# Kernel tuning notes

Measured on AMD Instinct MI355X. Metric: run time of the kernel, lower is better.

The kernel has to match this reference:

```python
import jax, jax.numpy as jnp
import numpy as np
import math

L = 2      # num_patient_encoder_layers
NE = 4     # number of note-type experts
H = 768    # hidden_size
FF = 4 * H # dim_feedforward
NH = H // 64  # num heads
HD = 64       # head dim
B, S = 8, 256
EPS = 1e-5


def setup_inputs() -> dict:
    key = jax.random.key(0)
    ks = jax.random.split(key, 12)
    std = 0.02
    x = jax.random.normal(ks[0], (B, S, H), dtype=jnp.float32)
    # all notes valid; note_pos values are 1..B*S so order_notes is an identity permutation
    note_pos = (jnp.arange(B * S, dtype=jnp.int64) + 1).reshape(B, S)
    note_type_pos = jax.random.randint(ks[1], (B * S,), 0, NE)
    Wq = jax.random.normal(ks[2], (L, H, H), dtype=jnp.float32) * std
    Wk = jax.random.normal(ks[3], (L, H, H), dtype=jnp.float32) * std
    Wv = jax.random.normal(ks[4], (L, H, H), dtype=jnp.float32) * std
    bq = jnp.zeros((L, H), jnp.float32)
    bk = jnp.zeros((L, H), jnp.float32)
    bv = jnp.zeros((L, H), jnp.float32)
    ln1_w = jnp.ones((L, H), jnp.float32)
    ln1_b = jnp.zeros((L, H), jnp.float32)
    ln2_w = jnp.ones((L, H), jnp.float32)
    ln2_b = jnp.zeros((L, H), jnp.float32)
    W1 = jax.random.normal(ks[5], (L, NE, H, FF), dtype=jnp.float32) * std
    b1 = jnp.zeros((L, NE, FF), jnp.float32)
    W2 = jax.random.normal(ks[6], (L, NE, FF, H), dtype=jnp.float32) * std
    b2 = jnp.zeros((L, NE, H), jnp.float32)
    return dict(x=x, note_pos=note_pos, note_type_pos=note_type_pos,
                Wq=Wq, bq=bq, Wk=Wk, bk=bk, Wv=Wv, bv=bv,
                ln1_w=ln1_w, ln1_b=ln1_b, ln2_w=ln2_w, ln2_b=ln2_b,
                W1=W1, b1=b1, W2=W2, b2=b2)


def _layer_norm(x, w, b):
    mu = jnp.mean(x, axis=-1, keepdims=True)
    var = jnp.mean(jnp.square(x - mu), axis=-1, keepdims=True)
    return (x - mu) * jax.lax.rsqrt(var + EPS) * w + b


def _sinusoidal_pe(seq_len, d_model):
    pos = jnp.arange(seq_len, dtype=jnp.float32)[:, None]
    div = jnp.exp(jnp.arange(0, d_model, 2, dtype=jnp.float32) * (-math.log(10000.0) / d_model))
    ang = pos * div  # [S, H/2]
    # interleave sin at even, cos at odd indices
    return jnp.stack([jnp.sin(ang), jnp.cos(ang)], axis=-1).reshape(seq_len, d_model)


def reference(x, note_pos, note_type_pos, Wq, bq, Wk, bk, Wv, bv,
              ln1_w, ln1_b, ln2_w, ln2_b, W1, b1, W2, b2):
    Bc, Sc, Hc = x.shape
    x = x + _sinusoidal_pe(Sc, Hc)[None]
    attn_mask = (note_pos != 0).astype(x.dtype)                 # [B, S]
    add_mask = (1.0 - attn_mask)[:, None, None, :] * -10000.0    # [B,1,1,S]
    flat_idx = note_pos.reshape(-1)                              # identity perm, values 1..B*S

    for l in range(L):
        # --- self attention (no 1/sqrt(d) scaling, as in source) ---
        h = _layer_norm(x, ln1_w[l], ln1_b[l])
        q = (h @ Wq[l] + bq[l]).reshape(Bc, Sc, NH, HD)
        k = (h @ Wk[l] + bk[l]).reshape(Bc, Sc, NH, HD)
        v = (h @ Wv[l] + bv[l]).reshape(Bc, Sc, NH, HD)
        scores = jnp.einsum('bqhd,bkhd->bhqk', q, k) + add_mask
        probs = jax.nn.softmax(scores, axis=-1)
        ctx = jnp.einsum('bhqk,bkhd->bqhd', probs, v).reshape(Bc, Sc, Hc)
        x = x + ctx

        # --- gather valid notes to flat token list (identity here) ---
        xf = x.reshape(-1, Hc)                                   # [T, H]
        hf = _layer_norm(xf, ln2_w[l], ln2_b[l])
        # --- note-type routed expert FFN ---
        out = jnp.zeros_like(xf)
        for e in range(NE):
            he = jax.nn.gelu(hf @ W1[l, e] + b1[l, e], approximate=False) @ W2[l, e] + b2[l, e]
            out = jnp.where((note_type_pos == e)[:, None], he, out)
        xf = xf + out
        # --- scatter back via order_notes: pad zero row, gather by note_pos ---
        padded = jnp.concatenate([jnp.zeros((1, Hc), xf.dtype), xf], axis=0)
        x = padded[flat_idx].reshape(Bc, Sc, Hc)
    return x
```

## Files before the change

### kernel.cpp

```cpp
#include <hip/hip_runtime.h>

typedef __bf16 bf16_t;
typedef __attribute__((ext_vector_type(8))) __bf16 bf16x8;
typedef __attribute__((ext_vector_type(4))) float f32x4;

static constexpr int Lc = 2, NEc = 4, Hc = 768, FFc = 3072, NHc = 12;
static constexpr int Bc = 8, Tc = 2048;

__device__ __forceinline__ void gll16(const bf16_t* g, bf16_t* l) {
  __builtin_amdgcn_global_load_lds(
      (const __attribute__((address_space(1))) void*)g,
      (__attribute__((address_space(3))) void*)l, 16, 0, 0);
}

__global__ __launch_bounds__(64) void route_k(const int* __restrict__ ntp,
                                              int* __restrict__ perm,
                                              int* __restrict__ offs) {
  int lane = threadIdx.x;
  int myE[32];
  int cnt0 = 0, cnt1 = 0, cnt2 = 0, cnt3 = 0;
  for (int c = 0; c < 32; ++c) {
    int e = ntp[c * 64 + lane];
    myE[c] = e;
    cnt0 += __popcll(__ballot(e == 0));
    cnt1 += __popcll(__ballot(e == 1));
    cnt2 += __popcll(__ballot(e == 2));
    cnt3 += __popcll(__ballot(e == 3));
  }
  int b0 = 0, b1 = cnt0, b2 = cnt0 + cnt1, b3 = cnt0 + cnt1 + cnt2;
  if (lane == 0) {
    offs[0] = 0; offs[1] = b1; offs[2] = b2; offs[3] = b3; offs[4] = b3 + cnt3;
  }
  unsigned long long below = (lane == 63) ? ~0ull >> 1 : ((1ull << lane) - 1);
  for (int c = 0; c < 32; ++c) {
    int e = myE[c];
    unsigned long long m0 = __ballot(e == 0), m1 = __ballot(e == 1);
    unsigned long long m2 = __ballot(e == 2), m3 = __ballot(e == 3);
    unsigned long long mm = (e == 0) ? m0 : (e == 1) ? m1 : (e == 2) ? m2 : m3;
    int base = (e == 0) ? b0 : (e == 1) ? b1 : (e == 2) ? b2 : b3;
    perm[base + __popcll(mm & below)] = c * 64 + lane;
    b0 += __popcll(m0); b1 += __popcll(m1); b2 += __popcll(m2); b3 += __popcll(m3);
  }
}

__global__ __launch_bounds__(256) void pe_add(const float* __restrict__ xin,
                                              float* __restrict__ x0) {
  int p = blockIdx.x * 256 + threadIdx.x;
  int t = p / 384;
  int jj = p - t * 384;
  int s = t & 255;
  float ang = (float)s * __expf((float)jj * -0.0239852613894f);
  float sn, cs;
  sincosf(ang, &sn, &cs);
  float2 xv = ((const float2*)xin)[p];
  float2 o;  o.x = xv.x + sn;  o.y = xv.y + cs;
  ((float2*)x0)[p] = o;
}

__global__ __launch_bounds__(256) void ln_k(const float* __restrict__ x,
                                            const float* __restrict__ g,
                                            const float* __restrict__ bb,
                                            bf16_t* __restrict__ out) {
  int w = threadIdx.x >> 6, lane = threadIdx.x & 63;
  int t = blockIdx.x * 4 + w;
  const float4* xr = (const float4*)(x + (size_t)t * Hc);
  float4 v[3];
  float s = 0.f, s2 = 0.f;
  for (int i = 0; i < 3; ++i) {
    v[i] = xr[lane + i * 64];
    s  += v[i].x + v[i].y + v[i].z + v[i].w;
    s2 += v[i].x * v[i].x + v[i].y * v[i].y + v[i].z * v[i].z + v[i].w * v[i].w;
  }
  for (int o = 1; o < 64; o <<= 1) { s += __shfl_xor(s, o); s2 += __shfl_xor(s2, o); }
  float mu = s * (1.f / 768.f);
  float r = rsqrtf(s2 * (1.f / 768.f) - mu * mu + 1e-5f);
  bf16_t* orow = out + (size_t)t * Hc;
  for (int i = 0; i < 3; ++i) {
    int i4 = lane + i * 64;
    float4 gg = ((const float4*)g)[i4];
    float4 b4 = ((const float4*)bb)[i4];
    union { bf16_t h[4]; uint2 u; } pk;
    pk.h[0] = (bf16_t)((v[i].x - mu) * r * gg.x + b4.x);
    pk.h[1] = (bf16_t)((v[i].y - mu) * r * gg.y + b4.y);
    pk.h[2] = (bf16_t)((v[i].z - mu) * r * gg.z + b4.z);
    pk.h[3] = (bf16_t)((v[i].w - mu) * r * gg.w + b4.w);
    ((uint2*)orow)[i4] = pk.u;
  }
}

__global__ __launch_bounds__(256) void tconv(const float* __restrict__ s0,
                                             const float* __restrict__ s1,
                                             const float* __restrict__ s2,
                                             int mdiv, long sls, long sms,
                                             bf16_t* __restrict__ dst, long dls, long dms,
                                             int K, int N) {
  int z = blockIdx.z;
  int l = z / mdiv, m = z % mdiv;
  const float* src;
  if (s1) src = (m == 0 ? s0 : (m == 1 ? s1 : s2)) + (size_t)l * sls;
  else src = s0 + (size_t)l * sls + (size_t)m * sms;
  bf16_t* d = dst + (size_t)l * dls + (size_t)m * dms;
  int n0 = blockIdx.x * 64, k0 = blockIdx.y * 64;
  __shared__ float tl[64][65];
  int c = threadIdx.x & 63, r0 = threadIdx.x >> 6;
  for (int i = 0; i < 16; ++i) {
    int r = r0 + i * 4;
    tl[r][c] = src[(size_t)(k0 + r) * N + n0 + c];
  }
  __syncthreads();
  for (int i = 0; i < 16; ++i) {
    int r = r0 + i * 4;
    d[(size_t)(n0 + r) * K + k0 + c] = (bf16_t)tl[c][r];
  }
}

template <int MODE, int BM>
__global__ __launch_bounds__(256) void gemm2(
    const bf16_t* __restrict__ A, const bf16_t* __restrict__ Bt,
    int K, int N, int kIters, long btStride, long biasStride,
    const int* __restrict__ perm, const int* __restrict__ offs,
    const float* __restrict__ bqp, const float* __restrict__ bkp,
    const float* __restrict__ bvp, const float* __restrict__ biasE,
    float* __restrict__ outF, bf16_t* __restrict__ outB) {
  constexpr int TM = BM / 32;
  constexpr int TN = 2;
  constexpr int AI = BM / 32;
  __shared__ bf16_t Ald[BM * 64];
  __shared__ bf16_t Bld[64 * 64];
  int tid = threadIdx.x, lane = tid & 63, w = tid >> 6;
  int quad = lane >> 4, col = lane & 15;
  int m0 = blockIdx.y * BM, n0 = blockIdx.x * 64;
  int e = 0, ks = 0, kStart = 0, off = 0, cnt = Tc;
  if (MODE == 1) e = blockIdx.z;
  if (MODE == 2) { e = blockIdx.z >> 1; ks = blockIdx.z & 1; kStart = ks * (K / 2); }
  if (MODE != 0) {
    off = offs[e];
    cnt = offs[e + 1] - off;
    if (m0 >= cnt) return;
  }
  const bf16_t* B0 = Bt + (size_t)e * btStride;

  const bf16_t* ga[AI];
  bf16_t* la[AI];
  for (int j = 0; j < AI; ++j) {
    int rbase = w * (BM / 4) + j * 8;
    int row = rbase + (lane >> 3);
    int ch = ((lane & 7) - row) & 7;
    int gm = m0 + row;
    int gmc = (gm < cnt) ? gm : (cnt - 1);
    int srow;
    if (MODE == 0) srow = gm;
    else if (MODE == 1) srow = perm[off + gmc];
    else srow = off + gmc;
    ga[j] = A + (size_t)srow * K + kStart + ch * 8;
    la[j] = Ald + rbase * 64;
  }
  const bf16_t* gb[2];
  bf16_t* lb[2];
  for (int j = 0; j < 2; ++j) {
    int rbase = w * 16 + j * 8;
    int row = rbase + (lane >> 3);
    int ch = ((lane & 7) - row) & 7;
    gb[j] = B0 + (size_t)(n0 + row) * K + kStart + ch * 8;
    lb[j] = Bld + rbase * 64;
  }

  int wr = (w >> 1) * (BM / 2), wc = (w & 1) * 32;
  int aoff[TM], boff[TN];
  for (int r = 0; r < TM; ++r) {
    int row = wr + r * 16 + col;
    aoff[r] = row * 64 + (((quad + row) & 7) << 3);
  }
  for (int c = 0; c < TN; ++c) {
    int row = wc + c * 16 + col;
    boff[c] = row * 64 + (((quad + row) & 7) << 3);
  }

  const f32x4 z4 = {0.f, 0.f, 0.f, 0.f};
  f32x4 acc[TM][TN];
  for (int r = 0; r < TM; ++r)
    for (int c = 0; c < TN; ++c) acc[r][c] = z4;

  for (int it = 0; it < kIters; ++it) {
    __syncthreads();
    for (int j = 0; j < AI; ++j) gll16(ga[j], la[j]);
    for (int j = 0; j < 2; ++j) gll16(gb[j], lb[j]);
    for (int j = 0; j < AI; ++j) ga[j] += 64;
    for (int j = 0; j < 2; ++j) gb[j] += 64;
    __syncthreads();
    for (int kk = 0; kk < 2; ++kk) {
      bf16x8 af[TM], bv[TN];
      for (int r = 0; r < TM; ++r) af[r] = *(const bf16x8*)(Ald + (aoff[r] ^ (kk << 5)));
      for (int c = 0; c < TN; ++c) bv[c] = *(const bf16x8*)(Bld + (boff[c] ^ (kk << 5)));
      for (int r = 0; r < TM; ++r)
        for (int c = 0; c < TN; ++c)
          acc[r][c] = __builtin_amdgcn_mfma_f32_16x16x32_bf16(af[r], bv[c], acc[r][c], 0, 0, 0);
    }
  }

  for (int r = 0; r < TM; ++r)
    for (int c = 0; c < TN; ++c) {
      int mloc = wr + r * 16 + quad * 4;
      int n = n0 + wc + c * 16 + col;
      for (int i = 0; i < 4; ++i) {
        int gm = m0 + mloc + i;
        float av = acc[r][c][i];
        if (MODE == 0) {
          float bias = (n < 768) ? bqp[n] : (n < 1536) ? bkp[n - 768] : bvp[n - 1536];
          outB[(size_t)gm * N + n] = (bf16_t)(av + bias);
        } else if (MODE == 1) {
          if (gm < cnt) {
            float v = av + biasE[(size_t)e * biasStride + n];
            float u = v * (0.7978845608f + 0.0356774081f * v * v);
            float t = 1.f - 2.f / (1.f + __expf(2.f * u));
            outB[(size_t)(off + gm) * N + n] = (bf16_t)(0.5f * v * (1.f + t));
          }
        } else {
          if (gm < cnt) {
            int tok = perm[off + gm];
            outF[(size_t)ks * Tc * Hc + (size_t)tok * N + n] = av;
          }
        }
      }
    }
}

__global__ __launch_bounds__(256) void attn_k(const bf16_t* __restrict__ qkv,
                                              const int* __restrict__ np,
                                              float* __restrict__ x) {
  __shared__ bf16_t Kld[256 * 64];
  __shared__ bf16_t Vt[64 * 256];
  int tid = threadIdx.x, lane = tid & 63, w = tid >> 6;
  int qt = blockIdx.x;
  int b = blockIdx.y / NHc, h = blockIdx.y % NHc;

  for (int j = 0; j < 8; ++j) {
    int rbase = w * 64 + j * 8;
    int row = rbase + (lane >> 3);
    int oc = ((lane & 7) - row) & 7;
    const bf16_t* gp = qkv + ((size_t)(b * 256 + row)) * 2304 + 768 + h * 64 + oc * 8;
    gll16(gp, Kld + rbase * 64);
  }
  {
    int s = tid, shi = s >> 3, slo = s & 7;
    const uint4* vs = (const uint4*)(qkv + ((size_t)(b * 256 + s)) * 2304 + 1536 + h * 64);
    for (int cc = 0; cc < 8; ++cc) {
      uint4 pk = vs[cc];
      const bf16_t* pv = (const bf16_t*)&pk;
      for (int jj = 0; jj < 8; ++jj) {
        int d = cc * 8 + jj;
        Vt[d * 256 + ((shi + d) & 31) * 8 + slo] = pv[jj];
      }
    }
  }
  int quad = lane >> 4, col = lane & 15;
  float madd[16];
  for (int nt = 0; nt < 16; ++nt)
    madd[nt] = (np[b * 256 + nt * 16 + col] != 0) ? 0.f : -10000.f;
  int qrow = qt * 64 + w * 16 + col;
  const bf16_t* qb = qkv + ((size_t)(b * 256 + qrow)) * 2304 + h * 64;
  bf16x8 qf0 = *(const bf16x8*)(qb + quad * 8);
  bf16x8 qf1 = *(const bf16x8*)(qb + 32 + quad * 8);
  __syncthreads();

  const f32x4 z4 = {0.f, 0.f, 0.f, 0.f};
  f32x4 sc[16];
  for (int nt = 0; nt < 16; ++nt) {
    int row = nt * 16 + col;
    bf16x8 k0 = *(const bf16x8*)(Kld + row * 64 + (((0 + quad + row) & 7) << 3));
    bf16x8 k1 = *(const bf16x8*)(Kld + row * 64 + (((4 + quad + row) & 7) << 3));
    f32x4 z = z4;
    z = __builtin_amdgcn_mfma_f32_16x16x32_bf16(qf0, k0, z, 0, 0, 0);
    z = __builtin_amdgcn_mfma_f32_16x16x32_bf16(qf1, k1, z, 0, 0, 0);
    sc[nt] = z;
  }
  for (int nt = 0; nt < 16; ++nt) {
    float a = madd[nt];
    sc[nt][0] += a; sc[nt][1] += a; sc[nt][2] += a; sc[nt][3] += a;
  }
  float pm[4], rl[4];
  for (int i = 0; i < 4; ++i) {
    float m = -1e30f;
    for (int nt = 0; nt < 16; ++nt) m = fmaxf(m, sc[nt][i]);
    for (int o = 1; o < 16; o <<= 1) m = fmaxf(m, __shfl_xor(m, o));
    float ssum = 0.f;
    for (int nt = 0; nt < 16; ++nt) ssum += __expf(sc[nt][i] - m);
    for (int o = 1; o < 16; o <<= 1) ssum += __shfl_xor(ssum, o);
    pm[i] = m;
    rl[i] = 1.f / ssum;
  }
  __syncthreads();
  bf16_t* Pb = Kld + w * 4096;
  for (int nt = 0; nt < 16; ++nt)
    for (int i = 0; i < 4; ++i) {
      int prow = quad * 4 + i;
      int key = nt * 16 + col;
      Pb[prow * 256 + (((key >> 3) + prow) & 31) * 8 + (key & 7)] =
          (bf16_t)__expf(sc[nt][i] - pm[i]);
    }
  __syncthreads();
  f32x4 oacc[4];
  for (int i = 0; i < 4; ++i) oacc[i] = z4;
  for (int kk2 = 0; kk2 < 8; ++kk2) {
    bf16x8 pa = *(const bf16x8*)(Pb + col * 256 + (((kk2 * 4 + quad + col) & 31) << 3));
    for (int nt2 = 0; nt2 < 4; ++nt2) {
      int d = nt2 * 16 + col;
      bf16x8 bv8 = *(const bf16x8*)(Vt + d * 256 + (((kk2 * 4 + quad + d) & 31) << 3));
      oacc[nt2] = __builtin_amdgcn_mfma_f32_16x16x32_bf16(pa, bv8, oacc[nt2], 0, 0, 0);
    }
  }
  for (int nt2 = 0; nt2 < 4; ++nt2)
    for (int i = 0; i < 4; ++i) {
      size_t o = ((size_t)(b * 256 + qt * 64 + w * 16 + quad * 4 + i)) * Hc + h * 64 + nt2 * 16 + col;
      x[o] += oacc[nt2][i] * rl[i];
    }
}

__global__ __launch_bounds__(256) void combine_k(const float* __restrict__ x0,
                                                 const float* __restrict__ pbuf,
                                                 const float* __restrict__ b2l,
                                                 const int* __restrict__ ntp,
                                                 const int* __restrict__ np,
                                                 float* __restrict__ dst) {
  int i = blockIdx.x * 256 + threadIdx.x;
  int t = i / 192, d = i - t * 192;
  int idx = np[t];
  float4 o;
  if (idx != 0) {
    int r = idx - 1;
    int e = ntp[r];
    size_t j = (size_t)r * 192 + d;
    float4 a = ((const float4*)x0)[j];
    float4 p0 = ((const float4*)pbuf)[j];
    float4 p1 = ((const float4*)pbuf)[(size_t)Tc * 192 + j];
    float4 bb = ((const float4*)(b2l + (size_t)e * Hc))[d];
    o.x = a.x + p0.x + p1.x + bb.x;
    o.y = a.y + p0.y + p1.y + bb.y;
    o.z = a.z + p0.z + p1.z + bb.z;
    o.w = a.w + p0.w + p1.w + bb.w;
  } else {
    o.x = o.y = o.z = o.w = 0.f;
  }
  ((float4*)dst)[i] = o;
}

extern "C" void kernel_launch(void* const* d_in, const int* in_sizes, int n_in,
                              void* d_out, int out_size, void* d_ws, size_t ws_size,
                              hipStream_t stream) {
  const float* x_in = (const float*)d_in[0];
  const int* note_pos = (const int*)d_in[1];
  const int* ntp = (const int*)d_in[2];
  const float* Wq = (const float*)d_in[3];
  const float* bq = (const float*)d_in[4];
  const float* Wk = (const float*)d_in[5];
  const float* bk = (const float*)d_in[6];
  const float* Wv = (const float*)d_in[7];
  const float* bv = (const float*)d_in[8];
  const float* ln1w = (const float*)d_in[9];
  const float* ln1b = (const float*)d_in[10];
  const float* ln2w = (const float*)d_in[11];
  const float* ln2b = (const float*)d_in[12];
  const float* W1 = (const float*)d_in[13];
  const float* b1 = (const float*)d_in[14];
  const float* W2 = (const float*)d_in[15];
  const float* b2 = (const float*)d_in[16];
  float* out = (float*)d_out;

  char* p = (char*)d_ws;
  auto carve = [&](size_t bytes) -> char* {
    char* r = p;
    p += (bytes + 255) & ~(size_t)255;
    return r;
  };
  float* xA = (float*)carve((size_t)Tc * Hc * 4);
  float* xB = (float*)carve((size_t)Tc * Hc * 4);
  float* pbuf = (float*)carve((size_t)2 * Tc * Hc * 4);
  bf16_t* h16 = (bf16_t*)carve((size_t)Tc * Hc * 2);
  bf16_t* big = (bf16_t*)carve((size_t)Tc * FFc * 2);
  bf16_t* qkv16 = big;
  bf16_t* act1 = big;
  bf16_t* wqkvt = (bf16_t*)carve((size_t)Lc * 2304 * 768 * 2);
  bf16_t* w1t = (bf16_t*)carve((size_t)Lc * NEc * FFc * Hc * 2);
  bf16_t* w2t = (bf16_t*)carve((size_t)Lc * NEc * Hc * FFc * 2);
  int* perm = (int*)carve(Tc * 4);
  int* offs = (int*)carve(64);

  route_k<<<1, 64, 0, stream>>>(ntp, perm, offs);
  pe_add<<<Tc * Hc / 2 / 256, 256, 0, stream>>>(x_in, xA);

  tconv<<<dim3(12, 12, 6), 256, 0, stream>>>(Wq, Wk, Wv, 3, (long)Hc * Hc, 0L,
                                             wqkvt, (long)2304 * 768, (long)Hc * Hc, Hc, Hc);
  tconv<<<dim3(48, 12, 8), 256, 0, stream>>>(W1, nullptr, nullptr, 4,
                                             (long)NEc * Hc * FFc, (long)Hc * FFc,
                                             w1t, (long)NEc * FFc * Hc, (long)FFc * Hc, Hc, FFc);
  tconv<<<dim3(12, 48, 8), 256, 0, stream>>>(W2, nullptr, nullptr, 4,
                                             (long)NEc * FFc * Hc, (long)FFc * Hc,
                                             w2t, (long)NEc * Hc * FFc, (long)Hc * FFc, FFc, Hc);

  float* xcur = xA;
  for (int l = 0; l < Lc; ++l) {
    float* xdst = (l == Lc - 1) ? out : xB;
    ln_k<<<Tc / 4, 256, 0, stream>>>(xcur, ln1w + l * Hc, ln1b + l * Hc, h16);
    gemm2<0, 128><<<dim3(36, 16, 1), 256, 0, stream>>>(
        h16, wqkvt + (size_t)l * 2304 * 768, Hc, 2304, 12, 0L, 0L, perm, offs,
        bq + l * Hc, bk + l * Hc, bv + l * Hc, nullptr, nullptr, qkv16);
    attn_k<<<dim3(4, Bc * NHc), 256, 0, stream>>>(qkv16, note_pos, xcur);
    ln_k<<<Tc / 4, 256, 0, stream>>>(xcur, ln2w + l * Hc, ln2b + l * Hc, h16);
    gemm2<1, 128><<<dim3(48, 16, NEc), 256, 0, stream>>>(
        h16, w1t + (size_t)l * NEc * FFc * Hc, Hc, FFc, 12, (long)FFc * Hc, (long)FFc,
        perm, offs, nullptr, nullptr, nullptr, b1 + (size_t)l * NEc * FFc, nullptr, act1);
    gemm2<2, 64><<<dim3(12, 32, NEc * 2), 256, 0, stream>>>(
        act1, w2t + (size_t)l * NEc * Hc * FFc, FFc, Hc, 24, (long)Hc * FFc, 0L,
        perm, offs, nullptr, nullptr, nullptr, nullptr, pbuf, nullptr);
    combine_k<<<Tc * 192 / 256, 256, 0, stream>>>(xcur, pbuf, b2 + (size_t)l * NEc * Hc,
                                                  ntp, note_pos, xdst);
    float* tmp = xcur; xcur = xdst; xB = tmp;
  }
}
```

Baseline: 454.6 us.

## Merge prep and weight-conversion launches and use 64-row GEMM tiles everywhere

Routing and positional-encoding add now share one kernel, with block 0 doing the routing. The three weight transpose-convert launches become one flat-grid kernel. The GEMM template drops the BM parameter and always uses 64x64 tiles, which doubles the grid for the QKV and FFN1 GEMMs. Fewer launches cut launch overhead, and smaller tiles give more blocks to fill the CUs, at the cost of less reuse per block and more redundant weight-tile loads.

```diff
diff --git a/kernel.cpp b/kernel.cpp
--- a/kernel.cpp
+++ b/kernel.cpp
@@ -13,39 +13,42 @@
       (__attribute__((address_space(3))) void*)l, 16, 0, 0);
 }
 
-__global__ __launch_bounds__(64) void route_k(const int* __restrict__ ntp,
+__global__ __launch_bounds__(256) void prep_k(const float* __restrict__ xin,
+                                              const int* __restrict__ ntp,
+                                              float* __restrict__ x0,
                                               int* __restrict__ perm,
                                               int* __restrict__ offs) {
-  int lane = threadIdx.x;
-  int myE[32];
-  int cnt0 = 0, cnt1 = 0, cnt2 = 0, cnt3 = 0;
-  for (int c = 0; c < 32; ++c) {
-    int e = ntp[c * 64 + lane];
-    myE[c] = e;
-    cnt0 += __popcll(__ballot(e == 0));
-    cnt1 += __popcll(__ballot(e == 1));
-    cnt2 += __popcll(__ballot(e == 2));
-    cnt3 += __popcll(__ballot(e == 3));
-  }
-  int b0 = 0, b1 = cnt0, b2 = cnt0 + cnt1, b3 = cnt0 + cnt1 + cnt2;
-  if (lane == 0) {
-    offs[0] = 0; offs[1] = b1; offs[2] = b2; offs[3] = b3; offs[4] = b3 + cnt3;
-  }
-  unsigned long long below = (lane == 63) ? ~0ull >> 1 : ((1ull << lane) - 1);
-  for (int c = 0; c < 32; ++c) {
-    int e = myE[c];
-    unsigned long long m0 = __ballot(e == 0), m1 = __ballot(e == 1);
-    unsigned long long m2 = __ballot(e == 2), m3 = __ballot(e == 3);
-    unsigned long long mm = (e == 0) ? m0 : (e == 1) ? m1 : (e == 2) ? m2 : m3;
-    int base = (e == 0) ? b0 : (e == 1) ? b1 : (e == 2) ? b2 : b3;
-    perm[base + __popcll(mm & below)] = c * 64 + lane;
-    b0 += __popcll(m0); b1 += __popcll(m1); b2 += __popcll(m2); b3 += __popcll(m3);
-  }
-}
-
-__global__ __launch_bounds__(256) void pe_add(const float* __restrict__ xin,
-                                              float* __restrict__ x0) {
-  int p = blockIdx.x * 256 + threadIdx.x;
+  if (blockIdx.x == 0) {
+    int tid = threadIdx.x;
+    if (tid >= 64) return;
+    int lane = tid;
+    int myE[32];
+    int cnt0 = 0, cnt1 = 0, cnt2 = 0, cnt3 = 0;
+    for (int c = 0; c < 32; ++c) {
+      int e = ntp[c * 64 + lane];
+      myE[c] = e;
+      cnt0 += __popcll(__ballot(e == 0));
+      cnt1 += __popcll(__ballot(e == 1));
+      cnt2 += __popcll(__ballot(e == 2));
+      cnt3 += __popcll(__ballot(e == 3));
+    }
+    int b0 = 0, b1 = cnt0, b2 = cnt0 + cnt1, b3 = cnt0 + cnt1 + cnt2;
+    if (lane == 0) {
+      offs[0] = 0; offs[1] = b1; offs[2] = b2; offs[3] = b3; offs[4] = b3 + cnt3;
+    }
+    unsigned long long below = (lane == 63) ? ~0ull >> 1 : ((1ull << lane) - 1);
+    for (int c = 0; c < 32; ++c) {
+      int e = myE[c];
+      unsigned long long m0 = __ballot(e == 0), m1 = __ballot(e == 1);
+      unsigned long long m2 = __ballot(e == 2), m3 = __ballot(e == 3);
+      unsigned long long mm = (e == 0) ? m0 : (e == 1) ? m1 : (e == 2) ? m2 : m3;
+      int base = (e == 0) ? b0 : (e == 1) ? b1 : (e == 2) ? b2 : b3;
+      perm[base + __popcll(mm & below)] = c * 64 + lane;
+      b0 += __popcll(m0); b1 += __popcll(m1); b2 += __popcll(m2); b3 += __popcll(m3);
+    }
+    return;
+  }
+  int p = (blockIdx.x - 1) * 256 + threadIdx.x;
   int t = p / 384;
   int jj = p - t * 384;
   int s = t & 255;
@@ -88,19 +91,40 @@
   }
 }
 
-__global__ __launch_bounds__(256) void tconv(const float* __restrict__ s0,
-                                             const float* __restrict__ s1,
-                                             const float* __restrict__ s2,
-                                             int mdiv, long sls, long sms,
-                                             bf16_t* __restrict__ dst, long dls, long dms,
-                                             int K, int N) {
-  int z = blockIdx.z;
-  int l = z / mdiv, m = z % mdiv;
+__global__ __launch_bounds__(256) void tconv_all(const float* __restrict__ Wq,
+                                                 const float* __restrict__ Wk,
+                                                 const float* __restrict__ Wv,
+                                                 const float* __restrict__ W1,
+                                                 const float* __restrict__ W2,
+                                                 bf16_t* __restrict__ wqkvt,
+                                                 bf16_t* __restrict__ w1t,
+                                                 bf16_t* __restrict__ w2t) {
+  int t = blockIdx.x;
   const float* src;
-  if (s1) src = (m == 0 ? s0 : (m == 1 ? s1 : s2)) + (size_t)l * sls;
-  else src = s0 + (size_t)l * sls + (size_t)m * sms;
-  bf16_t* d = dst + (size_t)l * dls + (size_t)m * dms;
-  int n0 = blockIdx.x * 64, k0 = blockIdx.y * 64;
+  bf16_t* d;
+  int K, N, n0, k0;
+  if (t < 864) {
+    int z = t / 144, r = t % 144;
+    int l = z / 3, m = z % 3;
+    src = (m == 0 ? Wq : (m == 1 ? Wk : Wv)) + (size_t)l * Hc * Hc;
+    d = wqkvt + (size_t)l * 2304 * 768 + (size_t)m * Hc * Hc;
+    K = 768; N = 768;
+    n0 = (r % 12) * 64; k0 = (r / 12) * 64;
+  } else if (t < 864 + 4608) {
+    t -= 864;
+    int z = t / 576, r = t % 576;
+    src = W1 + (size_t)z * Hc * FFc;
+    d = w1t + (size_t)z * FFc * Hc;
+    K = 768; N = 3072;
+    n0 = (r % 48) * 64; k0 = (r / 48) * 64;
+  } else {
+    t -= 864 + 4608;
+    int z = t / 576, r = t % 576;
+    src = W2 + (size_t)z * FFc * Hc;
+    d = w2t + (size_t)z * Hc * FFc;
+    K = 3072; N = 768;
+    n0 = (r % 12) * 64; k0 = (r / 12) * 64;
+  }
   __shared__ float tl[64][65];
   int c = threadIdx.x & 63, r0 = threadIdx.x >> 6;
   for (int i = 0; i < 16; ++i) {
@@ -114,7 +138,7 @@
   }
 }
 
-template <int MODE, int BM>
+template <int MODE>
 __global__ __launch_bounds__(256) void gemm2(
     const bf16_t* __restrict__ A, const bf16_t* __restrict__ Bt,
     int K, int N, int kIters, long btStride, long biasStride,
@@ -122,14 +146,11 @@
     const float* __restrict__ bqp, const float* __restrict__ bkp,
     const float* __restrict__ bvp, const float* __restrict__ biasE,
     float* __restrict__ outF, bf16_t* __restrict__ outB) {
-  constexpr int TM = BM / 32;
-  constexpr int TN = 2;
-  constexpr int AI = BM / 32;
-  __shared__ bf16_t Ald[BM * 64];
+  __shared__ bf16_t Ald[64 * 64];
   __shared__ bf16_t Bld[64 * 64];
   int tid = threadIdx.x, lane = tid & 63, w = tid >> 6;
   int quad = lane >> 4, col = lane & 15;
-  int m0 = blockIdx.y * BM, n0 = blockIdx.x * 64;
+  int m0 = blockIdx.y * 64, n0 = blockIdx.x * 64;
   int e = 0, ks = 0, kStart = 0, off = 0, cnt = Tc;
   if (MODE == 1) e = blockIdx.z;
   if (MODE == 2) { e = blockIdx.z >> 1; ks = blockIdx.z & 1; kStart = ks * (K / 2); }
@@ -140,10 +161,10 @@
   }
   const bf16_t* B0 = Bt + (size_t)e * btStride;
 
-  const bf16_t* ga[AI];
-  bf16_t* la[AI];
-  for (int j = 0; j < AI; ++j) {
-    int rbase = w * (BM / 4) + j * 8;
+  const bf16_t* ga[2];
+  bf16_t* la[2];
+  for (int j = 0; j < 2; ++j) {
+    int rbase = w * 16 + j * 8;
     int row = rbase + (lane >> 3);
     int ch = ((lane & 7) - row) & 7;
     int gm = m0 + row;
@@ -165,41 +186,42 @@
     lb[j] = Bld + rbase * 64;
   }
 
-  int wr = (w >> 1) * (BM / 2), wc = (w & 1) * 32;
-  int aoff[TM], boff[TN];
-  for (int r = 0; r < TM; ++r) {
+  int wr = (w >> 1) * 32, wc = (w & 1) * 32;
+  int aoff[2], boff[2];
+  for (int r = 0; r < 2; ++r) {
     int row = wr + r * 16 + col;
     aoff[r] = row * 64 + (((quad + row) & 7) << 3);
   }
-  for (int c = 0; c < TN; ++c) {
+  for (int c = 0; c < 2; ++c) {
     int row = wc + c * 16 + col;
     boff[c] = row * 64 + (((quad + row) & 7) << 3);
   }
 
   const f32x4 z4 = {0.f, 0.f, 0.f, 0.f};
-  f32x4 acc[TM][TN];
-  for (int r = 0; r < TM; ++r)
-    for (int c = 0; c < TN; ++c) acc[r][c] = z4;
+  f32x4 acc[2][2];
+  for (int r = 0; r < 2; ++r)
+    for (int c = 0; c < 2; ++c) acc[r][c] = z4;
 
   for (int it = 0; it < kIters; ++it) {
     __syncthreads();
-    for (int j = 0; j < AI; ++j) gll16(ga[j], la[j]);
-    for (int j = 0; j < 2; ++j) gll16(gb[j], lb[j]);
-    for (int j = 0; j < AI; ++j) ga[j] += 64;
-    for (int j = 0; j < 2; ++j) gb[j] += 64;
+    gll16(ga[0], la[0]);
+    gll16(ga[1], la[1]);
+    gll16(gb[0], lb[0]);
+    gll16(gb[1], lb[1]);
+    ga[0] += 64; ga[1] += 64; gb[0] += 64; gb[1] += 64;
     __syncthreads();
     for (int kk = 0; kk < 2; ++kk) {
-      bf16x8 af[TM], bv[TN];
-      for (int r = 0; r < TM; ++r) af[r] = *(const bf16x8*)(Ald + (aoff[r] ^ (kk << 5)));
-      for (int c = 0; c < TN; ++c) bv[c] = *(const bf16x8*)(Bld + (boff[c] ^ (kk << 5)));
-      for (int r = 0; r < TM; ++r)
-        for (int c = 0; c < TN; ++c)
+      bf16x8 af[2], bv[2];
+      for (int r = 0; r < 2; ++r) af[r] = *(const bf16x8*)(Ald + (aoff[r] ^ (kk << 5)));
+      for (int c = 0; c < 2; ++c) bv[c] = *(const bf16x8*)(Bld + (boff[c] ^ (kk << 5)));
+      for (int r = 0; r < 2; ++r)
+        for (int c = 0; c < 2; ++c)
           acc[r][c] = __builtin_amdgcn_mfma_f32_16x16x32_bf16(af[r], bv[c], acc[r][c], 0, 0, 0);
     }
   }
 
-  for (int r = 0; r < TM; ++r)
-    for (int c = 0; c < TN; ++c) {
+  for (int r = 0; r < 2; ++r)
+    for (int c = 0; c < 2; ++c) {
       int mloc = wr + r * 16 + quad * 4;
       int n = n0 + wc + c * 16 + col;
       for (int i = 0; i < 4; ++i) {
@@ -385,31 +407,22 @@
   int* perm = (int*)carve(Tc * 4);
   int* offs = (int*)carve(64);
 
-  route_k<<<1, 64, 0, stream>>>(ntp, perm, offs);
-  pe_add<<<Tc * Hc / 2 / 256, 256, 0, stream>>>(x_in, xA);
-
-  tconv<<<dim3(12, 12, 6), 256, 0, stream>>>(Wq, Wk, Wv, 3, (long)Hc * Hc, 0L,
-                                             wqkvt, (long)2304 * 768, (long)Hc * Hc, Hc, Hc);
-  tconv<<<dim3(48, 12, 8), 256, 0, stream>>>(W1, nullptr, nullptr, 4,
-                                             (long)NEc * Hc * FFc, (long)Hc * FFc,
-                                             w1t, (long)NEc * FFc * Hc, (long)FFc * Hc, Hc, FFc);
-  tconv<<<dim3(12, 48, 8), 256, 0, stream>>>(W2, nullptr, nullptr, 4,
-                                             (long)NEc * FFc * Hc, (long)FFc * Hc,
-                                             w2t, (long)NEc * Hc * FFc, (long)Hc * FFc, FFc, Hc);
+  prep_k<<<1 + Tc * Hc / 2 / 256, 256, 0, stream>>>(x_in, ntp, xA, perm, offs);
+  tconv_all<<<864 + 4608 + 4608, 256, 0, stream>>>(Wq, Wk, Wv, W1, W2, wqkvt, w1t, w2t);
 
   float* xcur = xA;
   for (int l = 0; l < Lc; ++l) {
     float* xdst = (l == Lc - 1) ? out : xB;
     ln_k<<<Tc / 4, 256, 0, stream>>>(xcur, ln1w + l * Hc, ln1b + l * Hc, h16);
-    gemm2<0, 128><<<dim3(36, 16, 1), 256, 0, stream>>>(
+    gemm2<0><<<dim3(36, 32, 1), 256, 0, stream>>>(
         h16, wqkvt + (size_t)l * 2304 * 768, Hc, 2304, 12, 0L, 0L, perm, offs,
         bq + l * Hc, bk + l * Hc, bv + l * Hc, nullptr, nullptr, qkv16);
     attn_k<<<dim3(4, Bc * NHc), 256, 0, stream>>>(qkv16, note_pos, xcur);
     ln_k<<<Tc / 4, 256, 0, stream>>>(xcur, ln2w + l * Hc, ln2b + l * Hc, h16);
-    gemm2<1, 128><<<dim3(48, 16, NEc), 256, 0, stream>>>(
+    gemm2<1><<<dim3(48, 32, NEc), 256, 0, stream>>>(
         h16, w1t + (size_t)l * NEc * FFc * Hc, Hc, FFc, 12, (long)FFc * Hc, (long)FFc,
         perm, offs, nullptr, nullptr, nullptr, b1 + (size_t)l * NEc * FFc, nullptr, act1);
-    gemm2<2, 64><<<dim3(12, 32, NEc * 2), 256, 0, stream>>>(
+    gemm2<2><<<dim3(12, 32, NEc * 2), 256, 0, stream>>>(
         act1, w2t + (size_t)l * NEc * Hc * FFc, FFc, Hc, 24, (long)Hc * FFc, 0L,
         perm, offs, nullptr, nullptr, nullptr, nullptr, pbuf, nullptr);
     combine_k<<<Tc * 192 / 256, 256, 0, stream>>>(xcur, pbuf, b2 + (size_t)l * NEc * Hc,
```

Result: no change. 447.7 us (-1.5%).
